# Performance work log

Measured on AMD Instinct MI355X. Metric: run time of the kernel, lower is better.

The kernel has to match this reference:

```python
import jax, jax.numpy as jnp
import numpy as np

CUTOFF_UPPER = 4.5
EYE3 = jnp.eye(3, dtype=jnp.float32)


def tensor_norm(t):
    return (t ** 2).sum((-2, -1))


def decompose_tensor(X):
    # X: [N, C, 3, 3]
    tr_mean = jnp.trace(X, axis1=-2, axis2=-1) / 3.0
    I = tr_mean[..., None, None] * EYE3
    Xt = jnp.swapaxes(X, -2, -1)
    A = 0.5 * (X - Xt)
    S = 0.5 * (X + Xt) - I
    return I, A, S


def chan_linear(T, W, b):
    # torch: Linear applied over the channel axis after permute(0,2,3,1)
    # T: [N, C, 3, 3], W: [C, C], b: [C]
    return jnp.einsum('nkij,ck->ncij', T, W) + b[None, :, None, None]


def setup_inputs() -> dict:
    key = jax.random.key(0)
    ks = jax.random.split(key, 16)
    Np1, H, R, E = 20001, 128, 64, 200000
    X = jax.random.normal(ks[0], (Np1, H, 3, 3), dtype=jnp.float32)
    edge_index = jax.random.randint(ks[1], (2, E), 0, Np1)
    edge_weight = jax.random.uniform(ks[2], (E,), dtype=jnp.float32) * CUTOFF_UPPER
    edge_attr = jax.random.normal(ks[3], (E, R), dtype=jnp.float32)
    s = lambda fin: 1.0 / np.sqrt(fin)
    W1 = jax.random.uniform(ks[4], (3, H, H), minval=-s(H), maxval=s(H), dtype=jnp.float32)
    b1 = jax.random.uniform(ks[5], (3, H), minval=-s(H), maxval=s(H), dtype=jnp.float32)
    W2a = jax.random.uniform(ks[6], (H, R), minval=-s(R), maxval=s(R), dtype=jnp.float32)
    b2a = jax.random.uniform(ks[7], (H,), minval=-s(R), maxval=s(R), dtype=jnp.float32)
    W2b = jax.random.uniform(ks[8], (2 * H, H), minval=-s(H), maxval=s(H), dtype=jnp.float32)
    b2b = jax.random.uniform(ks[9], (2 * H,), minval=-s(H), maxval=s(H), dtype=jnp.float32)
    W2c = jax.random.uniform(ks[10], (3 * H, 2 * H), minval=-s(2 * H), maxval=s(2 * H), dtype=jnp.float32)
    b2c = jax.random.uniform(ks[11], (3 * H,), minval=-s(2 * H), maxval=s(2 * H), dtype=jnp.float32)
    W3 = jax.random.uniform(ks[12], (3, H, H), minval=-s(H), maxval=s(H), dtype=jnp.float32)
    b3 = jax.random.uniform(ks[13], (3, H), minval=-s(H), maxval=s(H), dtype=jnp.float32)
    return dict(X=X, edge_index=edge_index, edge_weight=edge_weight, edge_attr=edge_attr,
                W1=W1, b1=b1, W2a=W2a, b2a=b2a, W2b=W2b, b2b=b2b, W2c=W2c, b2c=b2c, W3=W3, b3=b3)


def reference(X, edge_index, edge_weight, edge_attr, W1, b1, W2a, b2a, W2b, b2b, W2c, b2c, W3, b3):
    Np1, H = X.shape[0], X.shape[1]
    act = jax.nn.silu
    X = X / (tensor_norm(X) + 1.0)[..., None, None]
    I, A, S = decompose_tensor(X)
    I = chan_linear(I, W1[0], b1[0])
    A = chan_linear(A, W1[1], b1[1])
    S = chan_linear(S, W1[2], b1[2])
    Y = I + A + S
    h = act(edge_attr @ W2a.T + b2a)
    h = act(h @ W2b.T + b2b)
    h = act(h @ W2c.T + b2c)  # [E, 3H]
    C = 0.5 * (jnp.cos(edge_weight * (jnp.pi / CUTOFF_UPPER)) + 1.0)
    C = C * (edge_weight < CUTOFF_UPPER).astype(C.dtype)
    ea = (h * C[:, None]).reshape(h.shape[0], H, 3)
    dst, src = edge_index[0], edge_index[1]

    def mp(factor, T):
        msg = factor[:, :, None, None] * T[src]  # [E, H, 3, 3]
        return jax.ops.segment_sum(msg, dst, num_segments=Np1)

    msg = mp(ea[..., 0], I) + mp(ea[..., 1], A) + mp(ea[..., 2], S)
    new_features = jnp.matmul(msg, Y) + jnp.matmul(Y, msg)  # O(3) branch
    I, A, S = decompose_tensor(new_features)
    norm = (tensor_norm(I + A + S) + 1.0)[..., None, None]
    I, A, S = I / norm, A / norm, S / norm
    I = chan_linear(I, W3[0], b3[0])
    A = chan_linear(A, W3[1], b3[1])
    S = chan_linear(S, W3[2], b3[2])
    dX = I + A + S
    return X + dX + jnp.matmul(dX, dX)
```

## Files before the change

### kernel.cpp

```cpp
#include <hip/hip_runtime.h>
#include <math.h>
#include <stdint.h>

typedef unsigned short u16;
typedef __attribute__((ext_vector_type(8))) short short8;
typedef __attribute__((ext_vector_type(4))) float floatx4;

__device__ __forceinline__ float b2f(u16 u){
  union{unsigned int i; float f;} v; v.i = ((unsigned int)u)<<16; return v.f;
}
__device__ __forceinline__ u16 f2b(float f){
  union{unsigned int i; float f;} v; v.f = f;
  unsigned int r = (v.i + 0x7FFFu + ((v.i>>16)&1u))>>16;
  return (u16)r;
}
__device__ __forceinline__ float ldx(const void* p, size_t i, int isb){
  return isb ? b2f(((const u16*)p)[i]) : ((const float*)p)[i];
}
__device__ __forceinline__ void ldg16_bf(const u16* p, u16* o){
  uint4 v0 = *reinterpret_cast<const uint4*>(p);
  uint4 v1 = *reinterpret_cast<const uint4*>(p+8);
  unsigned int u[8] = {v0.x,v0.y,v0.z,v0.w,v1.x,v1.y,v1.z,v1.w};
#pragma unroll
  for (int i=0;i<8;i++){ o[2*i] = (u16)(u[i]&0xffffu); o[2*i+1] = (u16)(u[i]>>16); }
}
__device__ __forceinline__ void ldg16_f32(const float* p, u16* o){
#pragma unroll
  for (int i=0;i<4;i++){
    float4 v = reinterpret_cast<const float4*>(p)[i];
    o[4*i+0]=f2b(v.x); o[4*i+1]=f2b(v.y); o[4*i+2]=f2b(v.z); o[4*i+3]=f2b(v.w);
  }
}
__device__ __forceinline__ uint4 pack8(const u16* o){
  uint4 r;
  r.x = (unsigned int)o[0] | ((unsigned int)o[1]<<16);
  r.y = (unsigned int)o[2] | ((unsigned int)o[3]<<16);
  r.z = (unsigned int)o[4] | ((unsigned int)o[5]<<16);
  r.w = (unsigned int)o[6] | ((unsigned int)o[7]<<16);
  return r;
}

__global__ void k_sniff(const void* __restrict__ X, int* __restrict__ flag)
{
  __shared__ int cnt;
  if (threadIdx.x==0) cnt = 0;
  __syncthreads();
  int c = 0;
  for (int t = threadIdx.x; t < 512; t += 256){
    unsigned int u = ((const u16*)X)[2*t];
    int e = (u >> 7) & 0xFF;
    if (e >= 110 && e <= 139) c++;
  }
  atomicAdd(&cnt, c);
  __syncthreads();
  if (threadIdx.x==0) *flag = (cnt > 300) ? 1 : 0;
}

__global__ __launch_bounds__(256) void k_zero(float* __restrict__ p, int n)
{
  int i = blockIdx.x*256 + threadIdx.x;
  if (i < n) p[i] = 0.f;
}
__global__ __launch_bounds__(256) void k_zero_int(int* __restrict__ p, int n)
{
  int i = blockIdx.x*256 + threadIdx.x;
  if (i < n) p[i] = 0;
}

__global__ __launch_bounds__(256) void k_hist(
    const int* __restrict__ ei, int* __restrict__ counts, int E)
{
  int e = blockIdx.x*256 + threadIdx.x;
  if (e < E) atomicAdd(&counts[ei[e]], 1);
}
__global__ __launch_bounds__(256) void k_scan(
    const int* __restrict__ counts, int* __restrict__ rowptr,
    int* __restrict__ fill, int N)
{
  __shared__ int sm[256];
  __shared__ int carry;
  int tid = threadIdx.x;
  if (tid == 0) carry = 0;
  __syncthreads();
  for (int base = 0; base < N; base += 256){
    int v = (base+tid < N) ? counts[base+tid] : 0;
    sm[tid] = v;
    __syncthreads();
    for (int off=1; off<256; off<<=1){
      int t = (tid >= off) ? sm[tid-off] : 0;
      __syncthreads();
      sm[tid] += t;
      __syncthreads();
    }
    int excl = carry + sm[tid] - v;
    if (base+tid < N){ rowptr[base+tid] = excl; fill[base+tid] = excl; }
    __syncthreads();
    if (tid == 0) carry += sm[255];
    __syncthreads();
  }
  if (tid == 0) rowptr[N] = carry;
}
__global__ __launch_bounds__(256) void k_scatter(
    const int* __restrict__ ei, int* __restrict__ fill,
    int* __restrict__ eorder, int E)
{
  int e = blockIdx.x*256 + threadIdx.x;
  if (e >= E) return;
  int d = ei[e];
  int pos = atomicAdd(&fill[d], 1);
  eorder[pos] = e;
}

__global__ __launch_bounds__(256) void k_decompose(
    const void* __restrict__ X, u16* __restrict__ Di, u16* __restrict__ Da,
    u16* __restrict__ Ds, int NH, const int* __restrict__ dflag)
{
  int tid = blockIdx.x*256 + threadIdx.x;
  if (tid >= NH) return;
  int isb = *dflag;
  int n = tid >> 7, k = tid & 127;
  float x[9]; float nrm = 0.f;
#pragma unroll
  for (int i=0;i<9;i++){ x[i]=ldx(X,(size_t)tid*9+i,isb); nrm += x[i]*x[i]; }
  float inv = 1.0f/(nrm+1.0f);
#pragma unroll
  for (int i=0;i<9;i++) x[i]*=inv;
  float i0 = (x[0]+x[4]+x[8])*(1.0f/3.0f);
  Di[tid] = f2b(i0);
  size_t ab = ((size_t)n*3)*128 + k;
  Da[ab      ] = f2b(0.5f*(x[1]-x[3]));
  Da[ab + 128] = f2b(0.5f*(x[2]-x[6]));
  Da[ab + 256] = f2b(0.5f*(x[5]-x[7]));
  size_t sb = ((size_t)n*6)*128 + k;
  Ds[sb      ] = f2b(x[0]-i0);
  Ds[sb + 128] = f2b(0.5f*(x[1]+x[3]));
  Ds[sb + 256] = f2b(0.5f*(x[2]+x[6]));
  Ds[sb + 384] = f2b(x[4]-i0);
  Ds[sb + 512] = f2b(0.5f*(x[5]+x[7]));
  Ds[sb + 640] = f2b(x[8]-i0);
}

__global__ __launch_bounds__(256) void k_mfma_gemm(
    const void* __restrict__ A, size_t aoff, const int* __restrict__ rowidx, int ridx0,
    const void* __restrict__ Bw, size_t boff,
    const void* __restrict__ bias, const float* __restrict__ rowscale,
    u16* __restrict__ C, int M, int Ncol, int K, int flags,
    int aext, int bext, const int* __restrict__ dflag)
{
  __shared__ u16 AsU[128][40];
  __shared__ u16 BsU[128][40];
  int isb = *dflag;
  int isbA = aext ? isb : 1;
  int isbB = bext ? isb : 1;
  int tid = threadIdx.x;
  int lane = tid & 63, l15 = lane & 15, q = lane >> 4;
  int wid = tid >> 6, wm = wid & 1, wn = wid >> 1;
  int n0 = blockIdx.x * 128, m0 = blockIdx.y * 128;
  int r = tid >> 1, cs = (tid & 1) * 16;

  floatx4 acc[4][4];
#pragma unroll
  for (int i=0;i<4;i++)
#pragma unroll
    for (int j=0;j<4;j++) acc[i][j] = (floatx4)0.f;

  long arow = -1;
  {
    int gm = m0 + r;
    if (gm < M) arow = rowidx ? (long)rowidx[ridx0 + gm] : (long)gm;
  }
  int brow_g = n0 + r;
  int bsrc = (flags & 4) ? ((brow_g & 127)*3 + (brow_g >> 7)) : brow_g;

  for (int k0 = 0; k0 < K; k0 += 32){
    u16 ta[16], tb[16];
    if (arow >= 0){
      size_t base = aoff + (size_t)arow*K + k0 + cs;
      if (isbA) ldg16_bf((const u16*)A + base, ta);
      else      ldg16_f32((const float*)A + base, ta);
    } else {
#pragma unroll
      for (int i=0;i<16;i++) ta[i]=0;
    }
    {
      size_t base = boff + (size_t)bsrc*K + k0 + cs;
      if (isbB) ldg16_bf((const u16*)Bw + base, tb);
      else      ldg16_f32((const float*)Bw + base, tb);
    }
    __syncthreads();
    *reinterpret_cast<uint4*>(&AsU[r][cs])   = pack8(ta);
    *reinterpret_cast<uint4*>(&AsU[r][cs+8]) = pack8(ta+8);
    *reinterpret_cast<uint4*>(&BsU[r][cs])   = pack8(tb);
    *reinterpret_cast<uint4*>(&BsU[r][cs+8]) = pack8(tb+8);
    __syncthreads();
    short8 av[4], bv[4];
#pragma unroll
    for (int mt=0; mt<4; mt++)
      av[mt] = *reinterpret_cast<const short8*>(&AsU[wm*64 + mt*16 + l15][q*8]);
#pragma unroll
    for (int nt=0; nt<4; nt++)
      bv[nt] = *reinterpret_cast<const short8*>(&BsU[wn*64 + nt*16 + l15][q*8]);
#pragma unroll
    for (int mt=0; mt<4; mt++)
#pragma unroll
      for (int nt=0; nt<4; nt++)
        acc[mt][nt] = __builtin_amdgcn_mfma_f32_16x16x32_bf16(av[mt], bv[nt], acc[mt][nt], 0, 0, 0);
  }

  float biasv[4];
#pragma unroll
  for (int nt=0; nt<4; nt++){
    int col = n0 + wn*64 + nt*16 + l15;
    int bcol = (flags & 4) ? ((col & 127)*3 + (col >> 7)) : col;
    biasv[nt] = bias ? ldx(bias, bcol, isbB) : 0.f;
  }
#pragma unroll
  for (int mt=0; mt<4; mt++){
#pragma unroll
    for (int reg=0; reg<4; reg++){
      int row = m0 + wm*64 + mt*16 + q*4 + reg;
      if (row >= M) continue;
      float rs = (flags & 2) ? rowscale[row] : 1.0f;
#pragma unroll
      for (int nt=0; nt<4; nt++){
        int col = n0 + wn*64 + nt*16 + l15;
        float t = acc[mt][nt][reg] + biasv[nt];
        if (flags & 1) t = t / (1.0f + expf(-t));
        C[(size_t)row*Ncol + col] = f2b(t*rs);
      }
    }
  }
}

__global__ __launch_bounds__(256) void k_cutoff(
    const void* __restrict__ ew, const int* __restrict__ eorder, int c0,
    float* __restrict__ Cc, int ec, const int* __restrict__ dflag)
{
  int i = blockIdx.x*256 + threadIdx.x;
  if (i >= ec) return;
  int e = eorder[c0 + i];
  float w = ldx(ew, e, *dflag);
  float c = 0.0f;
  if (w < 4.5f) c = 0.5f*(cosf(w*0.6981317007977318f) + 1.0f);
  Cc[i] = c;
}

__global__ __launch_bounds__(128) void k_gather(
    const int* __restrict__ rowptr, const int* __restrict__ eorder,
    const int* __restrict__ ei, int E, int c0, int c1,
    const u16* __restrict__ ea,
    const u16* __restrict__ Pi, const u16* __restrict__ Pa,
    const u16* __restrict__ Ps, const void* __restrict__ b1,
    float* __restrict__ msg, int NH, const int* __restrict__ dflag)
{
  int n = blockIdx.x;
  int lo = rowptr[n], hi = rowptr[n+1];
  if (lo < c0) lo = c0;
  if (hi > c1) hi = c1;
  if (lo >= hi) return;
  int isb = *dflag;
  int c = threadIdx.x;
  float b0 = ldx(b1,c,isb), b1f = ldx(b1,128+c,isb), b2v = ldx(b1,256+c,isb);
  float m[9];
#pragma unroll
  for (int i=0;i<9;i++) m[i]=0.f;
  for (int idx = lo; idx < hi; idx++){
    int e = eorder[idx];
    int src = ei[E + e];
    const u16* er = ea + (size_t)(idx - c0)*384;
    float e0f = b2f(er[c]), e1f = b2f(er[128+c]), e2f = b2f(er[256+c]);
    float i1 = b2f(Pi[(size_t)src*128 + c]);
    size_t ab = (size_t)src*384 + c;
    float a0 = b2f(Pa[ab]), a1 = b2f(Pa[ab+128]), a2 = b2f(Pa[ab+256]);
    size_t sb = (size_t)src*768 + c;
    float s0 = b2f(Ps[sb]),     s1 = b2f(Ps[sb+128]), s2 = b2f(Ps[sb+256]);
    float s3 = b2f(Ps[sb+384]), s4 = b2f(Ps[sb+512]), s5 = b2f(Ps[sb+640]);
    float bb = e0f*b0 + e1f*b1f + e2f*b2v;
    float t0 = e0f*i1;
    m[0] += t0 + e2f*s0 + bb;
    m[1] += e1f*a0 + e2f*s1 + bb;
    m[2] += e1f*a1 + e2f*s2 + bb;
    m[3] += -e1f*a0 + e2f*s1 + bb;
    m[4] += t0 + e2f*s3 + bb;
    m[5] += e1f*a2 + e2f*s4 + bb;
    m[6] += -e1f*a1 + e2f*s2 + bb;
    m[7] += -e1f*a2 + e2f*s4 + bb;
    m[8] += t0 + e2f*s5 + bb;
  }
  size_t o = (size_t)n*128 + c;
#pragma unroll
  for (int i=0;i<9;i++) msg[(size_t)i*NH + o] += m[i];
}

__global__ __launch_bounds__(256) void k_update(
    const float* __restrict__ msg, const u16* __restrict__ Pi,
    const u16* __restrict__ Pa, const u16* __restrict__ Ps,
    const void* __restrict__ b1,
    u16* __restrict__ D2i, u16* __restrict__ D2a, u16* __restrict__ D2s,
    int NH, const int* __restrict__ dflag)
{
  int tid = blockIdx.x*256 + threadIdx.x;
  if (tid >= NH) return;
  int isb = *dflag;
  int n = tid >> 7, c = tid & 127;
  float Mx[9];
#pragma unroll
  for (int i=0;i<9;i++) Mx[i] = msg[(size_t)i*NH + tid];
  float i1 = b2f(Pi[tid]);
  size_t ab = ((size_t)n*3)*128 + c;
  float a0 = b2f(Pa[ab]), a1 = b2f(Pa[ab+128]), a2 = b2f(Pa[ab+256]);
  size_t sb = ((size_t)n*6)*128 + c;
  float s0 = b2f(Ps[sb]),     s1 = b2f(Ps[sb+128]), s2 = b2f(Ps[sb+256]);
  float s3 = b2f(Ps[sb+384]), s4 = b2f(Ps[sb+512]), s5 = b2f(Ps[sb+640]);
  float B = ldx(b1,c,isb) + ldx(b1,128+c,isb) + ldx(b1,256+c,isb);
  float Y[9];
  Y[0]= i1+s0+B; Y[1]= a0+s1+B; Y[2]= a1+s2+B;
  Y[3]=-a0+s1+B; Y[4]= i1+s3+B; Y[5]= a2+s4+B;
  Y[6]=-a1+s2+B; Y[7]=-a2+s4+B; Y[8]= i1+s5+B;
  float F[9];
#pragma unroll
  for (int i=0;i<3;i++)
#pragma unroll
    for (int j=0;j<3;j++){
      float acc = 0.f;
#pragma unroll
      for (int t=0;t<3;t++)
        acc += Mx[i*3+t]*Y[t*3+j] + Y[i*3+t]*Mx[t*3+j];
      F[i*3+j] = acc;
    }
  float nrm = 0.f;
#pragma unroll
  for (int i=0;i<9;i++) nrm += F[i]*F[i];
  float inv = 1.0f/(nrm+1.0f);
  float i2 = (F[0]+F[4]+F[8])*(1.0f/3.0f);
  D2i[tid] = f2b(i2*inv);
  D2a[ab      ] = f2b(0.5f*(F[1]-F[3])*inv);
  D2a[ab + 128] = f2b(0.5f*(F[2]-F[6])*inv);
  D2a[ab + 256] = f2b(0.5f*(F[5]-F[7])*inv);
  D2s[sb      ] = f2b((F[0]-i2)*inv);
  D2s[sb + 128] = f2b(0.5f*(F[1]+F[3])*inv);
  D2s[sb + 256] = f2b(0.5f*(F[2]+F[6])*inv);
  D2s[sb + 384] = f2b((F[4]-i2)*inv);
  D2s[sb + 512] = f2b(0.5f*(F[5]+F[7])*inv);
  D2s[sb + 640] = f2b((F[8]-i2)*inv);
}

__global__ __launch_bounds__(256) void k_final(
    const void* __restrict__ X, const u16* __restrict__ P2i,
    const u16* __restrict__ P2a, const u16* __restrict__ P2s,
    const void* __restrict__ b3, void* __restrict__ out, int NH,
    const int* __restrict__ dflag)
{
  int tid = blockIdx.x*256 + threadIdx.x;
  if (tid >= NH) return;
  int isb = *dflag;
  int n = tid >> 7, c = tid & 127;
  float i1 = b2f(P2i[tid]);
  size_t ab = ((size_t)n*3)*128 + c;
  float a0 = b2f(P2a[ab]), a1 = b2f(P2a[ab+128]), a2 = b2f(P2a[ab+256]);
  size_t sb = ((size_t)n*6)*128 + c;
  float s0 = b2f(P2s[sb]),     s1 = b2f(P2s[sb+128]), s2 = b2f(P2s[sb+256]);
  float s3 = b2f(P2s[sb+384]), s4 = b2f(P2s[sb+512]), s5 = b2f(P2s[sb+640]);
  float B = ldx(b3,c,isb) + ldx(b3,128+c,isb) + ldx(b3,256+c,isb);
  float dX[9];
  dX[0]= i1+s0+B; dX[1]= a0+s1+B; dX[2]= a1+s2+B;
  dX[3]=-a0+s1+B; dX[4]= i1+s3+B; dX[5]= a2+s4+B;
  dX[6]=-a1+s2+B; dX[7]=-a2+s4+B; dX[8]= i1+s5+B;

  float x[9]; float nrm = 0.f;
#pragma unroll
  for (int i=0;i<9;i++){ x[i]=ldx(X,(size_t)tid*9+i,isb); nrm += x[i]*x[i]; }
  float inv = 1.0f/(nrm+1.0f);

#pragma unroll
  for (int i=0;i<3;i++)
#pragma unroll
    for (int j=0;j<3;j++){
      float acc = 0.f;
#pragma unroll
      for (int t=0;t<3;t++) acc += dX[i*3+t]*dX[t*3+j];
      float v = x[i*3+j]*inv + dX[i*3+j] + acc;
      size_t oi = (size_t)tid*9 + i*3 + j;
      if (isb) ((u16*)out)[oi] = f2b(v);
      else     ((float*)out)[oi] = v;
    }
}

extern "C" void kernel_launch(void* const* d_in, const int* in_sizes, int n_in,
                              void* d_out, int out_size, void* d_ws, size_t ws_size,
                              hipStream_t stream)
{
  const void* X    = d_in[0];
  const int*  ei   = (const int*)d_in[1];
  const void* ew   = d_in[2];
  const void* eatt = d_in[3];
  const void* W1   = d_in[4];
  const void* b1   = d_in[5];
  const void* W2a  = d_in[6];
  const void* b2a  = d_in[7];
  const void* W2b  = d_in[8];
  const void* b2b  = d_in[9];
  const void* W2c  = d_in[10];
  const void* b2c  = d_in[11];
  const void* W3   = d_in[12];
  const void* b3   = d_in[13];

  const int NH = in_sizes[0]/9;
  const int E  = in_sizes[2];
  const int N  = NH/128;

  auto aln = [](size_t x){ return (x + 255) & ~(size_t)255; };
  char* ws = (char*)d_ws;
  size_t off = 0;
  size_t o_flag = off; off += 256;
  size_t o_msg  = off; off += aln((size_t)NH*9*4);
  size_t o_Di   = off; off += aln((size_t)NH*2);
  size_t o_Da   = off; off += aln((size_t)NH*6);
  size_t o_Ds   = off; off += aln((size_t)NH*12);
  size_t o_Pi   = off; off += aln((size_t)NH*2);
  size_t o_Pa   = off; off += aln((size_t)NH*6);
  size_t o_Ps   = off; off += aln((size_t)NH*12);
  size_t o_cnt  = off; off += aln((size_t)N*4);
  size_t o_rp   = off; off += aln((size_t)(N+1)*4);
  size_t o_fill = off; off += aln((size_t)N*4);
  size_t o_eord = off; off += aln((size_t)E*4);
  size_t persistent = off;

  int EC;
  {
    size_t avail = (ws_size > persistent + 4096) ? (ws_size - persistent - 4096) : 0;
    size_t ecmax = avail / 1540;
    if (ecmax > (size_t)E) ecmax = (size_t)E;
    EC = (int)(ecmax & ~(size_t)1023);
    if (EC < 1024) EC = 1024;
  }
  size_t o_h1 = persistent;
  size_t o_h2 = o_h1 + aln((size_t)EC*256);
  size_t o_ea = o_h2 + aln((size_t)EC*512);
  size_t o_Cc = o_ea + aln((size_t)EC*768);
  (void)n_in; (void)out_size;

  int* dflag = (int*)(ws + o_flag);
  u16* Di = (u16*)(ws + o_Di);
  u16* Da = (u16*)(ws + o_Da);
  u16* Ds = (u16*)(ws + o_Ds);
  u16* Pi = (u16*)(ws + o_Pi);
  u16* Pa = (u16*)(ws + o_Pa);
  u16* Ps = (u16*)(ws + o_Ps);
  float* msg = (float*)(ws + o_msg);
  int* counts = (int*)(ws + o_cnt);
  int* rowptr = (int*)(ws + o_rp);
  int* fill   = (int*)(ws + o_fill);
  int* eorder = (int*)(ws + o_eord);
  u16* h1 = (u16*)(ws + o_h1);
  u16* h2 = (u16*)(ws + o_h2);
  u16* ea = (u16*)(ws + o_ea);
  float* Cc = (float*)(ws + o_Cc);

  dim3 blk(256);
  auto gemm = [&](const void* A, size_t aoff, const int* ridx, int ridx0,
                  const void* Bw, size_t boff, const void* bias, const float* rs,
                  u16* C, int M, int Ncol, int K, int flags, int aext, int bext){
    dim3 grid(Ncol/128, (M+127)/128);
    k_mfma_gemm<<<grid, blk, 0, stream>>>(A, aoff, ridx, ridx0, Bw, boff, bias, rs,
                                          C, M, Ncol, K, flags, aext, bext, dflag);
  };

  k_sniff<<<1, blk, 0, stream>>>(X, dflag);
  k_decompose<<<(NH+255)/256, blk, 0, stream>>>(X, Di, Da, Ds, NH, dflag);
  gemm(Di, 0, nullptr, 0, W1, 0,     nullptr, nullptr, Pi, N,   128, 128, 0, 0, 1);
  gemm(Da, 0, nullptr, 0, W1, 16384, nullptr, nullptr, Pa, 3*N, 128, 128, 0, 0, 1);
  gemm(Ds, 0, nullptr, 0, W1, 32768, nullptr, nullptr, Ps, 6*N, 128, 128, 0, 0, 1);
  k_zero<<<((NH*9)+255)/256, blk, 0, stream>>>(msg, NH*9);
  k_zero_int<<<(N+255)/256, blk, 0, stream>>>(counts, N);
  k_hist<<<(E+255)/256, blk, 0, stream>>>(ei, counts, E);
  k_scan<<<1, blk, 0, stream>>>(counts, rowptr, fill, N);
  k_scatter<<<(E+255)/256, blk, 0, stream>>>(ei, fill, eorder, E);
  for (int c0 = 0; c0 < E; c0 += EC){
    int ec = E - c0; if (ec > EC) ec = EC;
    k_cutoff<<<(ec+255)/256, blk, 0, stream>>>(ew, eorder, c0, Cc, ec, dflag);
    gemm(eatt, 0, eorder, c0, W2a, 0, b2a, nullptr, h1, ec, 128, 64,  1, 1, 1);
    gemm(h1, 0, nullptr, 0,   W2b, 0, b2b, nullptr, h2, ec, 256, 128, 1, 0, 1);
    gemm(h2, 0, nullptr, 0,   W2c, 0, b2c, Cc,      ea, ec, 384, 256, 1|2|4, 0, 1);
    k_gather<<<N, dim3(128), 0, stream>>>(rowptr, eorder, ei, E, c0, c0+ec,
                                          ea, Pi, Pa, Ps, b1, msg, NH, dflag);
  }
  k_update<<<(NH+255)/256, blk, 0, stream>>>(msg, Pi, Pa, Ps, b1, Di, Da, Ds, NH, dflag);
  gemm(Di, 0, nullptr, 0, W3, 0,     nullptr, nullptr, Pi, N,   128, 128, 0, 0, 1);
  gemm(Da, 0, nullptr, 0, W3, 16384, nullptr, nullptr, Pa, 3*N, 128, 128, 0, 0, 1);
  gemm(Ds, 0, nullptr, 0, W3, 32768, nullptr, nullptr, Ps, 6*N, 128, 128, 0, 0, 1);
  k_final<<<(NH+255)/256, blk, 0, stream>>>(X, Pi, Pa, Ps, b3, d_out, NH, dflag);
}
```

Baseline: 1.003 ms.

## Use direct global-to-LDS loads in GEMM with pre-converted bf16 weights and permuted edge attrs

The GEMM now stages its A and B tiles with global_load_lds (16-byte direct-to-LDS loads) into an XOR-swizzled shared layout. This replaces the register round-trip, the per-element format checks and the row-index indirection. To make that possible, weights and biases are converted to bf16/fp32 once in new kernels, with the W2c row permutation baked in, and edge_attr is gathered into eorder order as bf16 up front. The cost is extra preprocessing kernels and workspace memory, plus a second barrier per k-step, since there is no double buffering.

```diff
diff --git a/kernel.cpp b/kernel.cpp
--- a/kernel.cpp
+++ b/kernel.cpp
@@ -17,27 +17,10 @@
 __device__ __forceinline__ float ldx(const void* p, size_t i, int isb){
   return isb ? b2f(((const u16*)p)[i]) : ((const float*)p)[i];
 }
-__device__ __forceinline__ void ldg16_bf(const u16* p, u16* o){
-  uint4 v0 = *reinterpret_cast<const uint4*>(p);
-  uint4 v1 = *reinterpret_cast<const uint4*>(p+8);
-  unsigned int u[8] = {v0.x,v0.y,v0.z,v0.w,v1.x,v1.y,v1.z,v1.w};
-#pragma unroll
-  for (int i=0;i<8;i++){ o[2*i] = (u16)(u[i]&0xffffu); o[2*i+1] = (u16)(u[i]>>16); }
-}
-__device__ __forceinline__ void ldg16_f32(const float* p, u16* o){
-#pragma unroll
-  for (int i=0;i<4;i++){
-    float4 v = reinterpret_cast<const float4*>(p)[i];
-    o[4*i+0]=f2b(v.x); o[4*i+1]=f2b(v.y); o[4*i+2]=f2b(v.z); o[4*i+3]=f2b(v.w);
-  }
-}
-__device__ __forceinline__ uint4 pack8(const u16* o){
-  uint4 r;
-  r.x = (unsigned int)o[0] | ((unsigned int)o[1]<<16);
-  r.y = (unsigned int)o[2] | ((unsigned int)o[3]<<16);
-  r.z = (unsigned int)o[4] | ((unsigned int)o[5]<<16);
-  r.w = (unsigned int)o[6] | ((unsigned int)o[7]<<16);
-  return r;
+__device__ __forceinline__ void gll16(const u16* g, u16* l){
+  __builtin_amdgcn_global_load_lds(
+      (const __attribute__((address_space(1))) unsigned int*)(g),
+      (__attribute__((address_space(3))) unsigned int*)(l), 16, 0, 0);
 }
 
 __global__ void k_sniff(const void* __restrict__ X, int* __restrict__ flag)
@@ -111,6 +94,50 @@
   eorder[pos] = e;
 }
 
+__global__ __launch_bounds__(256) void k_cvt_weights(
+    const void* __restrict__ W1, const void* __restrict__ W3,
+    const void* __restrict__ W2a, const void* __restrict__ W2b,
+    const void* __restrict__ W2c, u16* __restrict__ out,
+    const int* __restrict__ dflag)
+{
+  int isb = *dflag;
+  int i = blockIdx.x*256 + threadIdx.x;
+  if (i >= 237568) return;
+  float v;
+  if (i < 49152)        v = ldx(W1, i, isb);
+  else if (i < 98304)   v = ldx(W3, i-49152, isb);
+  else if (i < 106496)  v = ldx(W2a, i-98304, isb);
+  else if (i < 139264)  v = ldx(W2b, i-106496, isb);
+  else {
+    int j = i - 139264;
+    int r = j >> 8, c = j & 255;
+    v = ldx(W2c, (size_t)((r & 127)*3 + (r >> 7))*256 + c, isb);
+  }
+  out[i] = f2b(v);
+}
+__global__ __launch_bounds__(256) void k_cvt_biases(
+    const void* __restrict__ b2a, const void* __restrict__ b2b,
+    const void* __restrict__ b2c, float* __restrict__ out,
+    const int* __restrict__ dflag)
+{
+  int isb = *dflag;
+  int i = blockIdx.x*256 + threadIdx.x;
+  if (i < 128) out[i] = ldx(b2a, i, isb);
+  else if (i < 384) out[i] = ldx(b2b, i-128, isb);
+  else if (i < 768){ int c = i-384; out[i] = ldx(b2c, (c&127)*3 + (c>>7), isb); }
+}
+__global__ __launch_bounds__(256) void k_perm_eatt(
+    const void* __restrict__ eatt, const int* __restrict__ eorder,
+    u16* __restrict__ dst, int E, const int* __restrict__ dflag)
+{
+  int isb = *dflag;
+  int row = blockIdx.x*4 + (threadIdx.x >> 6);
+  int c = threadIdx.x & 63;
+  if (row >= E) return;
+  int e = eorder[row];
+  dst[(size_t)row*64 + c] = f2b(ldx(eatt, (size_t)e*64 + c, isb));
+}
+
 __global__ __launch_bounds__(256) void k_decompose(
     const void* __restrict__ X, u16* __restrict__ Di, u16* __restrict__ Da,
     u16* __restrict__ Ds, int NH, const int* __restrict__ dflag)
@@ -141,22 +168,27 @@
 }
 
 __global__ __launch_bounds__(256) void k_mfma_gemm(
-    const void* __restrict__ A, size_t aoff, const int* __restrict__ rowidx, int ridx0,
-    const void* __restrict__ Bw, size_t boff,
-    const void* __restrict__ bias, const float* __restrict__ rowscale,
-    u16* __restrict__ C, int M, int Ncol, int K, int flags,
-    int aext, int bext, const int* __restrict__ dflag)
-{
-  __shared__ u16 AsU[128][40];
-  __shared__ u16 BsU[128][40];
-  int isb = *dflag;
-  int isbA = aext ? isb : 1;
-  int isbB = bext ? isb : 1;
-  int tid = threadIdx.x;
-  int lane = tid & 63, l15 = lane & 15, q = lane >> 4;
-  int wid = tid >> 6, wm = wid & 1, wn = wid >> 1;
-  int n0 = blockIdx.x * 128, m0 = blockIdx.y * 128;
-  int r = tid >> 1, cs = (tid & 1) * 16;
+    const u16* __restrict__ A, const u16* __restrict__ B,
+    const float* __restrict__ bias, const float* __restrict__ rowscale,
+    u16* __restrict__ C, int M, int Ncol, int K, int flags)
+{
+  __shared__ u16 As[4096];
+  __shared__ u16 Bs[4096];
+  const int tid = threadIdx.x;
+  const int lane = tid & 63, l15 = lane & 15, q = lane >> 4;
+  const int wid = tid >> 6, wm = wid & 1, wn = wid >> 1;
+  const int n0 = blockIdx.x * 128, m0 = blockIdx.y * 128;
+
+  const int srow = wid*32 + (lane >> 2);
+  const int qsrc = (lane & 3) ^ ((lane >> 3) & 3);
+  int ar0 = m0 + srow;      if (ar0 >= M) ar0 = M-1;
+  int ar1 = m0 + srow + 16; if (ar1 >= M) ar1 = M-1;
+  const u16* aSrc0 = A + (size_t)ar0*K + qsrc*8;
+  const u16* aSrc1 = A + (size_t)ar1*K + qsrc*8;
+  const u16* bSrc0 = B + (size_t)(n0 + srow)*K + qsrc*8;
+  const u16* bSrc1 = B + (size_t)(n0 + srow + 16)*K + qsrc*8;
+  u16* aDst0 = &As[wid*1024];  u16* aDst1 = &As[wid*1024 + 512];
+  u16* bDst0 = &Bs[wid*1024];  u16* bDst1 = &Bs[wid*1024 + 512];
 
   floatx4 acc[4][4];
 #pragma unroll
@@ -164,56 +196,35 @@
 #pragma unroll
     for (int j=0;j<4;j++) acc[i][j] = (floatx4)0.f;
 
-  long arow = -1;
-  {
-    int gm = m0 + r;
-    if (gm < M) arow = rowidx ? (long)rowidx[ridx0 + gm] : (long)gm;
-  }
-  int brow_g = n0 + r;
-  int bsrc = (flags & 4) ? ((brow_g & 127)*3 + (brow_g >> 7)) : brow_g;
+  const int qsw  = ((q ^ ((l15 >> 1) & 3)) << 3);
+  const int aBase = (wm*64 + l15)*32 + qsw;
+  const int bBase = (wn*64 + l15)*32 + qsw;
 
   for (int k0 = 0; k0 < K; k0 += 32){
-    u16 ta[16], tb[16];
-    if (arow >= 0){
-      size_t base = aoff + (size_t)arow*K + k0 + cs;
-      if (isbA) ldg16_bf((const u16*)A + base, ta);
-      else      ldg16_f32((const float*)A + base, ta);
-    } else {
-#pragma unroll
-      for (int i=0;i<16;i++) ta[i]=0;
-    }
-    {
-      size_t base = boff + (size_t)bsrc*K + k0 + cs;
-      if (isbB) ldg16_bf((const u16*)Bw + base, tb);
-      else      ldg16_f32((const float*)Bw + base, tb);
-    }
-    __syncthreads();
-    *reinterpret_cast<uint4*>(&AsU[r][cs])   = pack8(ta);
-    *reinterpret_cast<uint4*>(&AsU[r][cs+8]) = pack8(ta+8);
-    *reinterpret_cast<uint4*>(&BsU[r][cs])   = pack8(tb);
-    *reinterpret_cast<uint4*>(&BsU[r][cs+8]) = pack8(tb+8);
+    gll16(aSrc0 + k0, aDst0);
+    gll16(aSrc1 + k0, aDst1);
+    gll16(bSrc0 + k0, bDst0);
+    gll16(bSrc1 + k0, bDst1);
     __syncthreads();
     short8 av[4], bv[4];
 #pragma unroll
     for (int mt=0; mt<4; mt++)
-      av[mt] = *reinterpret_cast<const short8*>(&AsU[wm*64 + mt*16 + l15][q*8]);
+      av[mt] = *reinterpret_cast<const short8*>(&As[aBase + mt*512]);
 #pragma unroll
     for (int nt=0; nt<4; nt++)
-      bv[nt] = *reinterpret_cast<const short8*>(&BsU[wn*64 + nt*16 + l15][q*8]);
+      bv[nt] = *reinterpret_cast<const short8*>(&Bs[bBase + nt*512]);
 #pragma unroll
     for (int mt=0; mt<4; mt++)
 #pragma unroll
       for (int nt=0; nt<4; nt++)
         acc[mt][nt] = __builtin_amdgcn_mfma_f32_16x16x32_bf16(av[mt], bv[nt], acc[mt][nt], 0, 0, 0);
+    __syncthreads();
   }
 
   float biasv[4];
 #pragma unroll
-  for (int nt=0; nt<4; nt++){
-    int col = n0 + wn*64 + nt*16 + l15;
-    int bcol = (flags & 4) ? ((col & 127)*3 + (col >> 7)) : col;
-    biasv[nt] = bias ? ldx(bias, bcol, isbB) : 0.f;
-  }
+  for (int nt=0; nt<4; nt++)
+    biasv[nt] = bias ? bias[n0 + wn*64 + nt*16 + l15] : 0.f;
 #pragma unroll
   for (int mt=0; mt<4; mt++){
 #pragma unroll
@@ -424,6 +435,9 @@
   size_t o_rp   = off; off += aln((size_t)(N+1)*4);
   size_t o_fill = off; off += aln((size_t)N*4);
   size_t o_eord = off; off += aln((size_t)E*4);
+  size_t o_eattb= off; off += aln((size_t)E*64*2);
+  size_t o_wb   = off; off += aln((size_t)237568*2);
+  size_t o_bf   = off; off += aln((size_t)768*4);
   size_t persistent = off;
 
   int EC;
@@ -452,42 +466,46 @@
   int* rowptr = (int*)(ws + o_rp);
   int* fill   = (int*)(ws + o_fill);
   int* eorder = (int*)(ws + o_eord);
+  u16* eattb  = (u16*)(ws + o_eattb);
+  u16* wb     = (u16*)(ws + o_wb);
+  float* bf   = (float*)(ws + o_bf);
   u16* h1 = (u16*)(ws + o_h1);
   u16* h2 = (u16*)(ws + o_h2);
   u16* ea = (u16*)(ws + o_ea);
   float* Cc = (float*)(ws + o_Cc);
 
   dim3 blk(256);
-  auto gemm = [&](const void* A, size_t aoff, const int* ridx, int ridx0,
-                  const void* Bw, size_t boff, const void* bias, const float* rs,
-                  u16* C, int M, int Ncol, int K, int flags, int aext, int bext){
+  auto gemm = [&](const u16* A, const u16* Bw, const float* bias, const float* rs,
+                  u16* C, int M, int Ncol, int K, int flags){
     dim3 grid(Ncol/128, (M+127)/128);
-    k_mfma_gemm<<<grid, blk, 0, stream>>>(A, aoff, ridx, ridx0, Bw, boff, bias, rs,
-                                          C, M, Ncol, K, flags, aext, bext, dflag);
+    k_mfma_gemm<<<grid, blk, 0, stream>>>(A, Bw, bias, rs, C, M, Ncol, K, flags);
   };
 
   k_sniff<<<1, blk, 0, stream>>>(X, dflag);
+  k_cvt_weights<<<(237568+255)/256, blk, 0, stream>>>(W1, W3, W2a, W2b, W2c, wb, dflag);
+  k_cvt_biases<<<3, blk, 0, stream>>>(b2a, b2b, b2c, bf, dflag);
   k_decompose<<<(NH+255)/256, blk, 0, stream>>>(X, Di, Da, Ds, NH, dflag);
-  gemm(Di, 0, nullptr, 0, W1, 0,     nullptr, nullptr, Pi, N,   128, 128, 0, 0, 1);
-  gemm(Da, 0, nullptr, 0, W1, 16384, nullptr, nullptr, Pa, 3*N, 128, 128, 0, 0, 1);
-  gemm(Ds, 0, nullptr, 0, W1, 32768, nullptr, nullptr, Ps, 6*N, 128, 128, 0, 0, 1);
+  gemm(Di, wb,       nullptr, nullptr, Pi, N,   128, 128, 0);
+  gemm(Da, wb+16384, nullptr, nullptr, Pa, 3*N, 128, 128, 0);
+  gemm(Ds, wb+32768, nullptr, nullptr, Ps, 6*N, 128, 128, 0);
   k_zero<<<((NH*9)+255)/256, blk, 0, stream>>>(msg, NH*9);
   k_zero_int<<<(N+255)/256, blk, 0, stream>>>(counts, N);
   k_hist<<<(E+255)/256, blk, 0, stream>>>(ei, counts, E);
   k_scan<<<1, blk, 0, stream>>>(counts, rowptr, fill, N);
   k_scatter<<<(E+255)/256, blk, 0, stream>>>(ei, fill, eorder, E);
+  k_perm_eatt<<<(E+3)/4, blk, 0, stream>>>(eatt, eorder, eattb, E, dflag);
   for (int c0 = 0; c0 < E; c0 += EC){
     int ec = E - c0; if (ec > EC) ec = EC;
     k_cutoff<<<(ec+255)/256, blk, 0, stream>>>(ew, eorder, c0, Cc, ec, dflag);
-    gemm(eatt, 0, eorder, c0, W2a, 0, b2a, nullptr, h1, ec, 128, 64,  1, 1, 1);
-    gemm(h1, 0, nullptr, 0,   W2b, 0, b2b, nullptr, h2, ec, 256, 128, 1, 0, 1);
-    gemm(h2, 0, nullptr, 0,   W2c, 0, b2c, Cc,      ea, ec, 384, 256, 1|2|4, 0, 1);
+    gemm(eattb + (size_t)c0*64, wb+98304,  bf,     nullptr, h1, ec, 128, 64,  1);
+    gemm(h1,                    wb+106496, bf+128, nullptr, h2, ec, 256, 128, 1);
+    gemm(h2,                    wb+139264, bf+384, Cc,      ea, ec, 384, 256, 1|2);
     k_gather<<<N, dim3(128), 0, stream>>>(rowptr, eorder, ei, E, c0, c0+ec,
                                           ea, Pi, Pa, Ps, b1, msg, NH, dflag);
   }
   k_update<<<(NH+255)/256, blk, 0, stream>>>(msg, Pi, Pa, Ps, b1, Di, Da, Ds, NH, dflag);
-  gemm(Di, 0, nullptr, 0, W3, 0,     nullptr, nullptr, Pi, N,   128, 128, 0, 0, 1);
-  gemm(Da, 0, nullptr, 0, W3, 16384, nullptr, nullptr, Pa, 3*N, 128, 128, 0, 0, 1);
-  gemm(Ds, 0, nullptr, 0, W3, 32768, nullptr, nullptr, Ps, 6*N, 128, 128, 0, 0, 1);
+  gemm(Di, wb+49152, nullptr, nullptr, Pi, N,   128, 128, 0);
+  gemm(Da, wb+65536, nullptr, nullptr, Pa, 3*N, 128, 128, 0);
+  gemm(Ds, wb+81920, nullptr, nullptr, Ps, 6*N, 128, 128, 0);
   k_final<<<(NH+255)/256, blk, 0, stream>>>(X, Pi, Pa, Ps, b3, d_out, NH, dflag);
 }
```

New measurement: 1.023 ms. 1.02x slower.
